# Optimization experiments

Measured on AMD Instinct MI355X. Metric: run time of the kernel, lower is better.

Reference implementation:

```python
import jax, jax.numpy as jnp
import numpy as np

BATCH, SEQ, DIM = 2, 2048, 1024
HEADS, HEAD_DIM = 16, 64
K_NEI = 64
SCALE = 1.0 / float(np.sqrt(HEAD_DIM))


def _cantor_routes(seq_len: int, k: int, depth: int = 8) -> np.ndarray:
    """Replicates _build_positional_routes: Cantor coords + topk smallest |ci-cj|."""
    pos = np.arange(seq_len, dtype=np.float64)
    x = pos / max(1, seq_len - 1)
    x = np.clip(x, 1e-6, 1.0 - 1e-6)
    val = np.zeros_like(x)
    factor = 0.5
    for _ in range(depth):
        xs = x * 3.0
        digit = np.floor(xs)
        x = xs - digit
        val = val + (digit == 2.0).astype(np.float64) * factor
        factor *= 0.5
    val = np.clip(val, 0.0, 1.0)
    dist = np.abs(val[:, None] - val[None, :])  # [S, S]
    routes = np.argsort(dist, axis=1, kind='stable')[:, :k]  # smallest-k neighbors
    return routes.astype(np.int32)


def setup_inputs() -> dict:
    key = jax.random.key(0)
    kx, kw1, kb1, kw2, kb2 = jax.random.split(key, 5)
    x = jax.random.normal(kx, (BATCH, SEQ, DIM), dtype=jnp.float32)
    qkv_w = jax.random.normal(kw1, (3 * DIM, DIM), dtype=jnp.float32) * 0.02
    qkv_b = jax.random.normal(kb1, (3 * DIM,), dtype=jnp.float32) * 0.02
    out_w = jax.random.normal(kw2, (DIM, DIM), dtype=jnp.float32) * 0.02
    out_b = jax.random.normal(kb2, (DIM,), dtype=jnp.float32) * 0.02
    routes = jnp.asarray(_cantor_routes(SEQ, K_NEI))  # [S, K] int32
    return {"x": x, "routes": routes, "qkv_w": qkv_w, "qkv_b": qkv_b,
            "out_w": out_w, "out_b": out_b}


def reference(x, routes, qkv_w, qkv_b, out_w, out_b):
    B, S, _ = x.shape
    # QKV projection (torch Linear: x @ W.T + b)
    qkv = x @ qkv_w.T + qkv_b                          # [B, S, 3*DIM]
    qkv = qkv.reshape(B, S, 3, HEADS, HEAD_DIM).transpose(2, 0, 3, 1, 4)
    q, k, v = qkv[0], qkv[1], qkv[2]                   # each [B, H, S, D]
    # Gather K/V along precomputed Cantor routes: [B, H, S, K, D]
    k_g = jnp.take(k, routes, axis=2)
    v_g = jnp.take(v, routes, axis=2)
    scores = jnp.einsum('bhqd,bhqkd->bhqk', q, k_g) * SCALE
    attn = jax.nn.softmax(scores, axis=-1)             # [B, H, S, K]
    out = jnp.einsum('bhqk,bhqkd->bhqd', attn, v_g)    # [B, H, S, D]
    out = out.transpose(0, 2, 1, 3).reshape(B, S, DIM)
    return out @ out_w.T + out_b
```

## Files before the change

### kernel.cpp

```cpp
#include <hip/hip_runtime.h>
#include <math.h>

#define BATCH    2
#define SEQ      2048
#define DIM      1024
#define HEADS    16
#define HEAD_DIM 64
#define K_NEI    64
#define QKV_DIM  3072
#define MROWS    (BATCH * SEQ)
#define ATT_SCALE 0.125f

typedef _Float16 half8  __attribute__((ext_vector_type(8)));
typedef _Float16 half4  __attribute__((ext_vector_type(4)));
typedef _Float16 half2t __attribute__((ext_vector_type(2)));
typedef float    floatx4 __attribute__((ext_vector_type(4)));

__device__ inline void async_copy16(const void* g, void* l) {
  __builtin_amdgcn_global_load_lds(
      (const __attribute__((address_space(1))) unsigned int*)g,
      (__attribute__((address_space(3))) unsigned int*)l, 16, 0, 0);
}

__device__ inline float dot2h(half2t a, half2t b, float c) {
#if defined(__has_builtin) && __has_builtin(__builtin_amdgcn_fdot2)
  return __builtin_amdgcn_fdot2(a, b, c, false);
#else
  return c + (float)a[0] * (float)b[0] + (float)a[1] * (float)b[1];
#endif
}

__global__ __launch_bounds__(256)
void cast3(const float* __restrict__ a, int na4,
           const float* __restrict__ b, int nb4,
           const float* __restrict__ c, int nc4,
           _Float16* __restrict__ oa, _Float16* __restrict__ ob,
           _Float16* __restrict__ oc) {
  const int total = na4 + nb4 + nc4;
  for (int i = blockIdx.x * blockDim.x + threadIdx.x; i < total;
       i += gridDim.x * blockDim.x) {
    const float* src; _Float16* dst; int idx;
    if (i < na4)            { src = a; dst = oa; idx = i; }
    else if (i < na4 + nb4) { src = b; dst = ob; idx = i - na4; }
    else                    { src = c; dst = oc; idx = i - na4 - nb4; }
    float4 v = *(const float4*)(src + (size_t)idx * 4);
    half4 o;
    o[0] = (_Float16)v.x; o[1] = (_Float16)v.y;
    o[2] = (_Float16)v.z; o[3] = (_Float16)v.w;
    *(half4*)(dst + (size_t)idx * 4) = o;
  }
}

template<int BM, int BN, bool HALF_OUT>
__global__ __launch_bounds__(256)
void gemm_bt_f16(const _Float16* __restrict__ A, const _Float16* __restrict__ B,
                 const float* __restrict__ bias, void* __restrict__ Cv,
                 int M, int N, int K) {
  constexpr int FI = BM / 32;
  constexpr int FJ = BN / 32;
  constexpr int CA = BM / 64;
  constexpr int CB = BN / 64;
  __shared__ _Float16 As[2 * BM * 32];
  __shared__ _Float16 Bs[2 * BN * 32];

  const int tid  = threadIdx.x;
  const int lane = tid & 63;
  const int w    = tid >> 6;
  const int wr   = w >> 1;
  const int wc   = w & 1;
  const int bm   = blockIdx.y * BM;
  const int bn   = blockIdx.x * BN;

  const int srow = w * 16 + (lane >> 2);
  const int scol = (lane & 3) * 8;
  const _Float16* ga = A + (size_t)(bm + srow) * K + scol;
  const _Float16* gb = B + (size_t)(bn + srow) * K + scol;

  const int frow = lane & 15;
  const int fk   = (lane >> 4) * 8;

  floatx4 acc[FI][FJ] = {};

  for (int k0 = 0; k0 < K; k0 += 64) {
#pragma unroll
    for (int sub = 0; sub < 2; sub++) {
      const int kk = k0 + sub * 32;
#pragma unroll
      for (int i = 0; i < CA; i++)
        async_copy16(ga + (size_t)(i * 64) * K + kk,
                     As + sub * BM * 32 + w * 512 + i * 2048);
#pragma unroll
      for (int i = 0; i < CB; i++)
        async_copy16(gb + (size_t)(i * 64) * K + kk,
                     Bs + sub * BN * 32 + w * 512 + i * 2048);
    }
    __syncthreads();

#pragma unroll
    for (int sub = 0; sub < 2; sub++) {
      half8 af[FI], bf[FJ];
#pragma unroll
      for (int i = 0; i < FI; i++)
        af[i] = *(const half8*)&As[sub * BM * 32 + (wr * (BM / 2) + i * 16 + frow) * 32 + fk];
#pragma unroll
      for (int j = 0; j < FJ; j++)
        bf[j] = *(const half8*)&Bs[sub * BN * 32 + (wc * (BN / 2) + j * 16 + frow) * 32 + fk];
#pragma unroll
      for (int i = 0; i < FI; i++)
#pragma unroll
        for (int j = 0; j < FJ; j++) {
          if (HALF_OUT)
            acc[i][j] = __builtin_amdgcn_mfma_f32_16x16x32_f16(bf[j], af[i], acc[i][j], 0, 0, 0);
          else
            acc[i][j] = __builtin_amdgcn_mfma_f32_16x16x32_f16(af[i], bf[j], acc[i][j], 0, 0, 0);
        }
    }
    __syncthreads();
  }

  if (HALF_OUT) {
    _Float16* C = (_Float16*)Cv;
    const int mloc = lane & 15;
    const int nloc = (lane >> 4) * 4;
#pragma unroll
    for (int j = 0; j < FJ; j++) {
      const int gcol = bn + wc * (BN / 2) + j * 16 + nloc;
      float4 bj = *(const float4*)(bias + gcol);
#pragma unroll
      for (int i = 0; i < FI; i++) {
        const int grow = bm + wr * (BM / 2) + i * 16 + mloc;
        half4 hv;
        hv[0] = (_Float16)(acc[i][j][0] + bj.x);
        hv[1] = (_Float16)(acc[i][j][1] + bj.y);
        hv[2] = (_Float16)(acc[i][j][2] + bj.z);
        hv[3] = (_Float16)(acc[i][j][3] + bj.w);
        *(half4*)(C + (size_t)grow * N + gcol) = hv;
      }
    }
  } else {
    float* C = (float*)Cv;
    const int crow = (lane >> 4) * 4;
    const int ccol = lane & 15;
#pragma unroll
    for (int j = 0; j < FJ; j++) {
      const int gcol = bn + wc * (BN / 2) + j * 16 + ccol;
      const float bj = bias[gcol];
#pragma unroll
      for (int i = 0; i < FI; i++) {
        const int grow = bm + wr * (BM / 2) + i * 16 + crow;
        float* cp = C + (size_t)grow * N + gcol;
#pragma unroll
        for (int r = 0; r < 4; r++)
          cp[(size_t)r * N] = acc[i][j][r] + bj;
      }
    }
  }
}

__global__ __launch_bounds__(256, 4)
void attn_kernel(const _Float16* __restrict__ qkv,
                 const int* __restrict__ routes,
                 _Float16* __restrict__ ao) {
  const int lane = threadIdx.x & 63;
  const int w    = threadIdx.x >> 6;
  const int g    = lane >> 4;
  const int c    = lane & 15;

  const int i    = blockIdx.x;
  const int xcd  = i & 7;
  const int j    = i >> 3;
  const int bh   = j >> 6;
  const int qsub = j & 63;
  const int qblk = xcd * 64 + qsub;
  const int q    = qblk * 4 + w;
  const int h    = bh & 15;
  const int b    = bh >> 4;

  const size_t row_base = (size_t)b * SEQ;
  const int    hoff     = h * HEAD_DIM;

  const int rt = routes[q * K_NEI + lane];

  const half4 qv = *(const half4*)(qkv + (row_base + q) * QKV_DIM + hoff + 4 * c);
  const half2t qv01 = { qv[0], qv[1] };
  const half2t qv23 = { qv[2], qv[3] };

  float  s_reg[16];
  half4  vv[16];

#pragma unroll
  for (int t = 0; t < 16; t++) {
    const int ri = __shfl(rt, 4 * t + g);
    const _Float16* kp = qkv + (row_base + ri) * QKV_DIM + DIM + hoff + 4 * c;
    half4 kv = *(const half4*)kp;
    vv[t]    = *(const half4*)(kp + DIM);
    half2t k01 = { kv[0], kv[1] };
    half2t k23 = { kv[2], kv[3] };
    float sp = dot2h(k23, qv23, dot2h(k01, qv01, 0.f));
#pragma unroll
    for (int off = 1; off < 16; off <<= 1) sp += __shfl_xor(sp, off);
    s_reg[t] = sp;
  }

  float m = s_reg[0];
#pragma unroll
  for (int t = 1; t < 16; t++) m = fmaxf(m, s_reg[t]);
  m = fmaxf(m, __shfl_xor(m, 16));
  m = fmaxf(m, __shfl_xor(m, 32));

  float sum = 0.f;
#pragma unroll
  for (int t = 0; t < 16; t++) {
    s_reg[t] = __expf((s_reg[t] - m) * ATT_SCALE);
    sum += s_reg[t];
  }
  sum += __shfl_xor(sum, 16);
  sum += __shfl_xor(sum, 32);
  const float rinv = 1.f / sum;

  float o0 = 0.f, o1 = 0.f, o2 = 0.f, o3 = 0.f;
#pragma unroll
  for (int t = 0; t < 16; t++) {
    const float p = s_reg[t] * rinv;
    o0 += p * (float)vv[t][0];
    o1 += p * (float)vv[t][1];
    o2 += p * (float)vv[t][2];
    o3 += p * (float)vv[t][3];
  }
  o0 += __shfl_xor(o0, 16); o0 += __shfl_xor(o0, 32);
  o1 += __shfl_xor(o1, 16); o1 += __shfl_xor(o1, 32);
  o2 += __shfl_xor(o2, 16); o2 += __shfl_xor(o2, 32);
  o3 += __shfl_xor(o3, 16); o3 += __shfl_xor(o3, 32);

  if (g == 0) {
    half4 hv;
    hv[0] = (_Float16)o0; hv[1] = (_Float16)o1;
    hv[2] = (_Float16)o2; hv[3] = (_Float16)o3;
    *(half4*)(ao + (row_base + q) * DIM + hoff + 4 * c) = hv;
  }
}

extern "C" void kernel_launch(void* const* d_in, const int* in_sizes, int n_in,
                              void* d_out, int out_size, void* d_ws, size_t ws_size,
                              hipStream_t stream) {
  const float* x      = (const float*)d_in[0];
  const int*   routes = (const int*)  d_in[1];
  const float* qkv_w  = (const float*)d_in[2];
  const float* qkv_b  = (const float*)d_in[3];
  const float* out_w  = (const float*)d_in[4];
  const float* out_b  = (const float*)d_in[5];
  float* out = (float*)d_out;

  _Float16* qkvh = (_Float16*)d_ws;
  _Float16* aoh  = qkvh + (size_t)MROWS * QKV_DIM;
  _Float16* xh   = aoh  + (size_t)MROWS * DIM;
  _Float16* wh   = xh   + (size_t)MROWS * DIM;
  _Float16* owh  = wh   + (size_t)QKV_DIM * DIM;

  cast3<<<1024, 256, 0, stream>>>(x, MROWS * DIM / 4,
                                  qkv_w, QKV_DIM * DIM / 4,
                                  out_w, DIM * DIM / 4,
                                  xh, wh, owh);

  {
    dim3 g(QKV_DIM / 128, MROWS / 128);
    gemm_bt_f16<128, 128, true><<<g, 256, 0, stream>>>(xh, wh, qkv_b, qkvh,
                                                       MROWS, QKV_DIM, DIM);
  }

  attn_kernel<<<(BATCH * HEADS * SEQ) / 4, 256, 0, stream>>>(qkvh, routes, aoh);

  {
    dim3 g(DIM / 128, MROWS / 64);
    gemm_bt_f16<64, 128, false><<<g, 256, 0, stream>>>(aoh, owh, out_b, out,
                                                       MROWS, DIM, DIM);
  }
}
```

Baseline: 211.3 us.

## Replace per-score shuffle reductions in attention with LDS transpose reduction

The attention kernel now writes the 16 partial dot products per lane to a per-wave LDS scratch and reads them back transposed, so each lane reduces one full score with vector loads. This replaces 16x4 cross-lane shuffles with a single LDS round-trip, and softmax then runs one score per lane. Routes are loaded directly per lane instead of via shuffles, and the occupancy hint in launch bounds is dropped. It relies on intra-wave LDS ordering without barriers and adds LDS usage per block.

```diff
diff --git a/kernel.cpp b/kernel.cpp
--- a/kernel.cpp
+++ b/kernel.cpp
@@ -157,7 +157,7 @@
   }
 }
 
-__global__ __launch_bounds__(256, 4)
+__global__ __launch_bounds__(256)
 void attn_kernel(const _Float16* __restrict__ qkv,
                  const int* __restrict__ routes,
                  _Float16* __restrict__ ao) {
@@ -176,52 +176,56 @@
   const int h    = bh & 15;
   const int b    = bh >> 4;
 
+  __shared__ float scratch[4][16 * 68];
+  float* sw = scratch[w];
+
   const size_t row_base = (size_t)b * SEQ;
   const int    hoff     = h * HEAD_DIM;
 
-  const int rt = routes[q * K_NEI + lane];
+  const int* rbase = routes + q * K_NEI + g;
+  int rq[16];
+#pragma unroll
+  for (int t = 0; t < 16; t++) rq[t] = rbase[4 * t];
 
   const half4 qv = *(const half4*)(qkv + (row_base + q) * QKV_DIM + hoff + 4 * c);
   const half2t qv01 = { qv[0], qv[1] };
   const half2t qv23 = { qv[2], qv[3] };
 
-  float  s_reg[16];
-  half4  vv[16];
+  half4 vv[16];
 
 #pragma unroll
   for (int t = 0; t < 16; t++) {
-    const int ri = __shfl(rt, 4 * t + g);
-    const _Float16* kp = qkv + (row_base + ri) * QKV_DIM + DIM + hoff + 4 * c;
+    const _Float16* kp = qkv + (row_base + rq[t]) * QKV_DIM + DIM + hoff + 4 * c;
     half4 kv = *(const half4*)kp;
     vv[t]    = *(const half4*)(kp + DIM);
     half2t k01 = { kv[0], kv[1] };
     half2t k23 = { kv[2], kv[3] };
     float sp = dot2h(k23, qv23, dot2h(k01, qv01, 0.f));
-#pragma unroll
-    for (int off = 1; off < 16; off <<= 1) sp += __shfl_xor(sp, off);
-    s_reg[t] = sp;
-  }
-
-  float m = s_reg[0];
-#pragma unroll
-  for (int t = 1; t < 16; t++) m = fmaxf(m, s_reg[t]);
-  m = fmaxf(m, __shfl_xor(m, 16));
-  m = fmaxf(m, __shfl_xor(m, 32));
-
-  float sum = 0.f;
+    sw[t * 68 + lane] = sp;
+  }
+
+  const int rb = (lane >> 2) * 68 + (lane & 3) * 16;
+  float4 p0 = *(const float4*)&sw[rb];
+  float4 p1 = *(const float4*)&sw[rb + 4];
+  float4 p2 = *(const float4*)&sw[rb + 8];
+  float4 p3 = *(const float4*)&sw[rb + 12];
+  float sc = ((p0.x + p0.y) + (p0.z + p0.w)) + ((p1.x + p1.y) + (p1.z + p1.w))
+           + ((p2.x + p2.y) + (p2.z + p2.w)) + ((p3.x + p3.y) + (p3.z + p3.w));
+
+  float m = sc;
+#pragma unroll
+  for (int off = 1; off < 64; off <<= 1) m = fmaxf(m, __shfl_xor(m, off));
+  float e = __expf((sc - m) * ATT_SCALE);
+  float sum = e;
+#pragma unroll
+  for (int off = 1; off < 64; off <<= 1) sum += __shfl_xor(sum, off);
+  const float pn = e / sum;
+
+  sw[lane] = pn;
+  float o0 = 0.f, o1 = 0.f, o2 = 0.f, o3 = 0.f;
 #pragma unroll
   for (int t = 0; t < 16; t++) {
-    s_reg[t] = __expf((s_reg[t] - m) * ATT_SCALE);
-    sum += s_reg[t];
-  }
-  sum += __shfl_xor(sum, 16);
-  sum += __shfl_xor(sum, 32);
-  const float rinv = 1.f / sum;
-
-  float o0 = 0.f, o1 = 0.f, o2 = 0.f, o3 = 0.f;
-#pragma unroll
-  for (int t = 0; t < 16; t++) {
-    const float p = s_reg[t] * rinv;
+    const float p = sw[4 * t + g];
     o0 += p * (float)vv[t][0];
     o1 += p * (float)vv[t][1];
     o2 += p * (float)vv[t][2];
```

New measurement: 208.7 us (median of 2 runs). No clear change (-1.2%).
